# Kernel optimization log

Measured on AMD Instinct MI355X. Metric: run time of the kernel, lower is better.

## Reference

```python
import jax, jax.numpy as jnp
import numpy as np

NUM_HEADS = 8


def setup_inputs() -> dict:
    key = jax.random.key(0)
    ks = jax.random.split(key, 6)
    B, E, L = 8, 256, 4096
    top_k = 256
    return {
        "query": jax.random.normal(ks[0], (B, E, L), jnp.float32),
        "keys": jax.random.normal(ks[1], (B, E, L), jnp.float32),
        "values": jax.random.normal(ks[2], (B, E, L), jnp.float32),
        "rand_token_ind": jax.random.randint(ks[3], (B, top_k), 0, L),
        "in_proj_weight": jax.random.normal(ks[4], (3 * E, E), jnp.float32) / np.float32(np.sqrt(E)),
        "in_proj_bias": jnp.zeros((3 * E,), jnp.float32),
        "out_proj_weight": jax.random.normal(ks[5], (E, E), jnp.float32) / np.float32(np.sqrt(E)),
        "out_proj_bias": jnp.zeros((E,), jnp.float32),
        "top_k": top_k,
    }


def _forward(query, keys, values, rand_token_ind, in_proj_weight, in_proj_bias,
             out_proj_weight, out_proj_bias, top_k):
    B, E, Lq = query.shape
    # flatten(2).transpose(-1,-2): channel-first -> [B, L, E]
    q = jnp.swapaxes(query, 1, 2)
    k = jnp.swapaxes(keys, 1, 2)
    v = jnp.swapaxes(values, 1, 2)

    # --- dist_to_random_Q_selection ---
    # random subset of queries, [B, S, E]
    Q_small = jnp.take_along_axis(q, rand_token_ind[:, :, None], axis=1)

    # running min over subset queries of L1 distance (avoids [B,Lk,S,D] blowup)
    def step(min_d, qs):  # qs: [B, E]
        d = jnp.sum(jnp.abs(k - qs[:, None, :]), axis=-1)  # [B, Lk]
        return jnp.minimum(min_d, d), None

    init = jnp.full((B, k.shape[1]), jnp.inf, dtype=k.dtype)
    min_d, _ = jax.lax.scan(step, init, jnp.swapaxes(Q_small, 0, 1))

    # top_k smallest distances, sorted ascending (torch largest=False, sorted=True)
    _, idx = jax.lax.top_k(-min_d, top_k)  # idx: [B, top_k]
    sk = jnp.take_along_axis(k, idx[:, :, None], axis=1)  # [B, top_k, E]
    sv = jnp.take_along_axis(v, idx[:, :, None], axis=1)

    # --- standard torch MultiheadAttention (batch_first) ---
    Wq, Wk, Wv = jnp.split(in_proj_weight, 3, axis=0)
    bq, bk, bv = jnp.split(in_proj_bias, 3, axis=0)
    hd = E // NUM_HEADS
    scale = hd ** -0.5

    def heads(x):
        return x.reshape(x.shape[0], x.shape[1], NUM_HEADS, hd)

    qh = heads(q @ Wq.T + bq) * scale      # [B, Lq, H, hd]
    kh = heads(sk @ Wk.T + bk)             # [B, K,  H, hd]
    vh = heads(sv @ Wv.T + bv)

    scores = jnp.einsum('bqhd,bkhd->bhqk', qh, kh)
    attn = jax.nn.softmax(scores, axis=-1)
    o = jnp.einsum('bhqk,bkhd->bqhd', attn, vh).reshape(B, Lq, E)
    out = o @ out_proj_weight.T + out_proj_bias  # [B, Lq, E]

    # transpose back to original [B, E, Lq] layout
    return jnp.swapaxes(out, 1, 2)


def reference(query, keys, values, rand_token_ind, in_proj_weight, in_proj_bias,
              out_proj_weight, out_proj_bias, top_k):
    return _forward(query, keys, values, rand_token_ind, in_proj_weight,
                    in_proj_bias, out_proj_weight, out_proj_bias, top_k)
```

## Files before the change

### kernel.cpp

```cpp
#include <hip/hip_runtime.h>
#include <math.h>

#define B_SZ   8
#define E_DIM  256
#define L_SEQ  4096
#define S_TOP  256
#define NHEAD  8
#define HD     32
#define NSPLIT 4
#define JSPL   8

typedef __attribute__((ext_vector_type(8))) short bf16x8;
typedef __attribute__((ext_vector_type(4))) float f32x4;

__device__ inline short f2bf(float x) {
    union { float f; unsigned u; } v; v.f = x;
    unsigned r = (v.u + 0x7fff + ((v.u >> 16) & 1)) >> 16;
    return (short)r;
}

__global__ __launch_bounds__(256) void k_gather(const float* __restrict__ query,
                                                const int* __restrict__ ind,
                                                float* __restrict__ qs_pack) {
    int t = blockIdx.x * 256 + threadIdx.x;
    int e = t & (E_DIM - 1);
    int s = (t >> 8) & (S_TOP - 1);
    int b = t >> 16;
    int idx = ind[b * S_TOP + s];
    qs_pack[t] = query[((size_t)b * E_DIM + e) * L_SEQ + idx];
}

__global__ __launch_bounds__(256) void k_dist(const float* __restrict__ keys,
                                              const float* __restrict__ qs_pack,
                                              double* __restrict__ minpart) {
    const int b  = blockIdx.z;
    const int ss = blockIdx.y;
    const int l0 = blockIdx.x * 64;
    const int lid = threadIdx.x;
    const int tx = lid & 15;
    const int ty = lid >> 4;
    __shared__ float Ks[32][64];
    __shared__ float Qs[64][36];
    double (*red)[64] = (double(*)[64])&Ks[0][0];

    const float* kb = keys + (size_t)b * E_DIM * L_SEQ + l0;
    const float* qb = qs_pack + ((size_t)b * S_TOP + ss * 64) * E_DIM;

    double d[4][4];
#pragma unroll
    for (int i = 0; i < 4; ++i)
#pragma unroll
        for (int j = 0; j < 4; ++j) d[i][j] = 0.0;

    for (int c0 = 0; c0 < E_DIM; c0 += 32) {
        __syncthreads();
#pragma unroll
        for (int r = 0; r < 2; ++r) {
            int f4 = lid + 256 * r;
            int e  = f4 >> 4, l4 = (f4 & 15) * 4;
            *(float4*)&Ks[e][l4] = *(const float4*)(kb + (size_t)(c0 + e) * L_SEQ + l4);
            int s  = f4 >> 3, e4 = (f4 & 7) * 4;
            *(float4*)&Qs[s][e4] = *(const float4*)(qb + (size_t)s * E_DIM + c0 + e4);
        }
        __syncthreads();

        float cs[4][4] = {};
#pragma unroll
        for (int e4 = 0; e4 < 32; e4 += 4) {
            float qv[4][4];
#pragma unroll
            for (int j = 0; j < 4; ++j) {
                float4 q = *(const float4*)&Qs[ty * 4 + j][e4];
                qv[j][0] = q.x; qv[j][1] = q.y; qv[j][2] = q.z; qv[j][3] = q.w;
            }
#pragma unroll
            for (int ee = 0; ee < 4; ++ee) {
                float kv[4];
#pragma unroll
                for (int i = 0; i < 4; ++i) kv[i] = Ks[e4 + ee][tx * 4 + i];
#pragma unroll
                for (int i = 0; i < 4; ++i)
#pragma unroll
                    for (int j = 0; j < 4; ++j)
                        cs[i][j] += fabsf(kv[i] - qv[j][ee]);
            }
        }
#pragma unroll
        for (int i = 0; i < 4; ++i)
#pragma unroll
            for (int j = 0; j < 4; ++j) d[i][j] += (double)cs[i][j];
    }

    double md[4];
#pragma unroll
    for (int i = 0; i < 4; ++i) {
        double m = d[i][0];
        m = fmin(m, d[i][1]);
        m = fmin(m, d[i][2]);
        m = fmin(m, d[i][3]);
        md[i] = m;
    }
    __syncthreads();
#pragma unroll
    for (int i = 0; i < 4; ++i) red[ty][tx * 4 + i] = md[i];
    __syncthreads();
    if (lid < 64) {
        double m = red[0][lid];
#pragma unroll
        for (int t = 1; t < 16; ++t) m = fmin(m, red[t][lid]);
        minpart[((size_t)(b * NSPLIT + ss)) * L_SEQ + l0 + lid] = m;
    }
}

__global__ __launch_bounds__(256) void k_rankpart(const double* __restrict__ minpart,
                                                  int* __restrict__ rankpart) {
    const int b  = blockIdx.z;
    const int js = blockIdx.y;
    const int l  = blockIdx.x * 256 + threadIdx.x;
    __shared__ double sd[512];
    const double* mp = minpart + (size_t)b * NSPLIT * L_SEQ;
    for (int jj = threadIdx.x; jj < 512; jj += 256) {
        const int j = js * 512 + jj;
        double v = mp[j];
        v = fmin(v, mp[L_SEQ + j]);
        v = fmin(v, mp[2 * L_SEQ + j]);
        v = fmin(v, mp[3 * L_SEQ + j]);
        sd[jj] = v;
    }
    double dl = mp[l];
    dl = fmin(dl, mp[L_SEQ + l]);
    dl = fmin(dl, mp[2 * L_SEQ + l]);
    dl = fmin(dl, mp[3 * L_SEQ + l]);
    __syncthreads();
    const int jbase = js * 512;
    int rank = 0;
#pragma unroll 8
    for (int jj = 0; jj < 512; ++jj) {
        double dj = sd[jj];
        rank += (dj < dl) || (dj == dl && (jbase + jj) < l) ? 1 : 0;
    }
    rankpart[((size_t)(b * JSPL + js)) * L_SEQ + l] = rank;
}

__global__ __launch_bounds__(256) void k_sel(const int* __restrict__ rankpart,
                                             int* __restrict__ sel) {
    const int t = blockIdx.x * 256 + threadIdx.x;
    const int b = t >> 12;
    const int l = t & (L_SEQ - 1);
    int r = 0;
#pragma unroll
    for (int s = 0; s < JSPL; ++s)
        r += rankpart[((size_t)(b * JSPL + s)) * L_SEQ + l];
    if (r < S_TOP) sel[b * S_TOP + r] = l;
}

__global__ __launch_bounds__(256) void k_kvproj2(const float* __restrict__ keys,
                                                 const float* __restrict__ vals,
                                                 const int* __restrict__ sel,
                                                 const float* __restrict__ Wk,
                                                 const float* __restrict__ bk,
                                                 const float* __restrict__ Wv,
                                                 const float* __restrict__ bv,
                                                 short* __restrict__ khb,
                                                 short* __restrict__ vtb) {
    const int b  = blockIdx.z;
    const int f0 = blockIdx.x * 64;
    const int TR = blockIdx.y >> 2;
    const int k0 = (blockIdx.y & 3) * 64;
    const float* src  = TR ? vals : keys;
    const float* W    = TR ? Wv : Wk;
    const float* bias = TR ? bv : bk;
    const int tx = threadIdx.x, ty = threadIdx.y;
    const int lid = ty * 16 + tx;
    __shared__ float As[16][68];
    __shared__ float Ws[16][68];
    float c[4][4] = {};
    const float* sb = src + (size_t)b * E_DIM * L_SEQ;
    const int* selb = sel + b * S_TOP;
    for (int e0 = 0; e0 < E_DIM; e0 += 16) {
        {
            int e  = lid >> 4;
            int k4 = (lid & 15) * 4;
#pragma unroll
            for (int c2 = 0; c2 < 4; ++c2) {
                int kk = k4 + c2;
                As[e][kk] = sb[(size_t)(e0 + e) * L_SEQ + selb[k0 + kk]];
            }
        }
        {
            int f  = lid >> 2;
            int e4 = (lid & 3) * 4;
            float4 w = *(const float4*)(W + (size_t)(f0 + f) * E_DIM + e0 + e4);
            Ws[e4 + 0][f] = w.x; Ws[e4 + 1][f] = w.y;
            Ws[e4 + 2][f] = w.z; Ws[e4 + 3][f] = w.w;
        }
        __syncthreads();
#pragma unroll
        for (int e = 0; e < 16; ++e) {
            float4 a = *(const float4*)&As[e][ty * 4];
            float4 w = *(const float4*)&Ws[e][tx * 4];
            float av[4] = {a.x, a.y, a.z, a.w};
            float wv[4] = {w.x, w.y, w.z, w.w};
#pragma unroll
            for (int i = 0; i < 4; ++i)
#pragma unroll
                for (int j = 0; j < 4; ++j) c[i][j] += av[i] * wv[j];
        }
        __syncthreads();
    }
    if (TR == 0) {
#pragma unroll
        for (int i = 0; i < 4; ++i) {
            short4 o;
            o.x = f2bf(c[i][0] + bias[f0 + tx * 4 + 0]);
            o.y = f2bf(c[i][1] + bias[f0 + tx * 4 + 1]);
            o.z = f2bf(c[i][2] + bias[f0 + tx * 4 + 2]);
            o.w = f2bf(c[i][3] + bias[f0 + tx * 4 + 3]);
            *(short4*)(khb + ((size_t)b * S_TOP + k0 + ty * 4 + i) * E_DIM + f0 + tx * 4) = o;
        }
    } else {
#pragma unroll
        for (int j = 0; j < 4; ++j) {
            const float bvv = bias[f0 + tx * 4 + j];
            short4 o;
            o.x = f2bf(c[0][j] + bvv); o.y = f2bf(c[1][j] + bvv);
            o.z = f2bf(c[2][j] + bvv); o.w = f2bf(c[3][j] + bvv);
            *(short4*)(vtb + ((size_t)b * E_DIM + f0 + tx * 4 + j) * S_TOP + k0 + ty * 4) = o;
        }
    }
}

__global__ __launch_bounds__(256) void k_qproj(const float* __restrict__ query,
                                               const float* __restrict__ W,
                                               const float* __restrict__ bias,
                                               short* __restrict__ qhb,
                                               float scale) {
    const int b  = blockIdx.z;
    const int f0 = blockIdx.x * 128;
    const int l0 = blockIdx.y * 128;
    const int tx = threadIdx.x, ty = threadIdx.y;
    const int lid = ty * 16 + tx;
    __shared__ float As[16][132];
    __shared__ float Ws[16][132];
    float c[8][8] = {};
    const float* sb = query + (size_t)b * E_DIM * L_SEQ + l0;
    for (int e0 = 0; e0 < E_DIM; e0 += 16) {
        __syncthreads();
#pragma unroll
        for (int r = 0; r < 2; ++r) {
            int f4 = lid + 256 * r;
            int e  = f4 >> 5, l4 = (f4 & 31) * 4;
            *(float4*)&As[e][l4] = *(const float4*)(sb + (size_t)(e0 + e) * L_SEQ + l4);
            int f  = f4 >> 2, e4 = (f4 & 3) * 4;
            float4 w = *(const float4*)(W + (size_t)(f0 + f) * E_DIM + e0 + e4);
            Ws[e4 + 0][f] = w.x; Ws[e4 + 1][f] = w.y;
            Ws[e4 + 2][f] = w.z; Ws[e4 + 3][f] = w.w;
        }
        __syncthreads();
#pragma unroll
        for (int e = 0; e < 16; ++e) {
            float4 a0 = *(const float4*)&As[e][tx * 4];
            float4 a1 = *(const float4*)&As[e][64 + tx * 4];
            float4 w0 = *(const float4*)&Ws[e][ty * 4];
            float4 w1 = *(const float4*)&Ws[e][64 + ty * 4];
            float av[8] = {a0.x, a0.y, a0.z, a0.w, a1.x, a1.y, a1.z, a1.w};
            float wv[8] = {w0.x, w0.y, w0.z, w0.w, w1.x, w1.y, w1.z, w1.w};
#pragma unroll
            for (int i = 0; i < 8; ++i)
#pragma unroll
                for (int j = 0; j < 8; ++j) c[i][j] += av[i] * wv[j];
        }
    }
    float bv[8];
#pragma unroll
    for (int j = 0; j < 8; ++j)
        bv[j] = bias[f0 + ((j < 4) ? ty * 4 + j : 64 + ty * 4 + (j - 4))];
#pragma unroll
    for (int i = 0; i < 8; ++i) {
        const int l = l0 + ((i < 4) ? tx * 4 + i : 64 + tx * 4 + (i - 4));
        short* row = qhb + ((size_t)b * L_SEQ + l) * E_DIM + f0;
        short4 o0, o1;
        o0.x = f2bf(scale * (c[i][0] + bv[0]));
        o0.y = f2bf(scale * (c[i][1] + bv[1]));
        o0.z = f2bf(scale * (c[i][2] + bv[2]));
        o0.w = f2bf(scale * (c[i][3] + bv[3]));
        o1.x = f2bf(scale * (c[i][4] + bv[4]));
        o1.y = f2bf(scale * (c[i][5] + bv[5]));
        o1.z = f2bf(scale * (c[i][6] + bv[6]));
        o1.w = f2bf(scale * (c[i][7] + bv[7]));
        *(short4*)(row + ty * 4) = o0;
        *(short4*)(row + 64 + ty * 4) = o1;
    }
}

__global__ __launch_bounds__(256) void k_attn(const short* __restrict__ qhb,
                                              const short* __restrict__ khb,
                                              const short* __restrict__ vtb,
                                              float* __restrict__ ob) {
    __shared__ short P[4][16][264];
    const int b = blockIdx.z, h = blockIdx.y;
    const int wv   = threadIdx.x >> 6;
    const int lane = threadIdx.x & 63;
    const int quad = lane >> 4;
    const int m    = lane & 15;
    const int l0 = blockIdx.x * 64 + wv * 16;

    const short* qp = qhb + ((size_t)b * L_SEQ + l0 + m) * E_DIM + h * HD + quad * 8;
    const bf16x8 qa = *(const bf16x8*)qp;

    const short* kb = khb + (size_t)b * S_TOP * E_DIM + h * HD + quad * 8;
    f32x4 sacc[16];
    const f32x4 zero = {0.f, 0.f, 0.f, 0.f};
#pragma unroll
    for (int t = 0; t < 16; ++t) {
        bf16x8 kf = *(const bf16x8*)(kb + (size_t)(t * 16 + m) * E_DIM);
        sacc[t] = __builtin_amdgcn_mfma_f32_16x16x32_bf16(qa, kf, zero, 0, 0, 0);
    }

    float mx[4], ssum[4];
#pragma unroll
    for (int r = 0; r < 4; ++r) {
        float v = sacc[0][r];
#pragma unroll
        for (int t = 1; t < 16; ++t) v = fmaxf(v, sacc[t][r]);
#pragma unroll
        for (int off = 1; off < 16; off <<= 1) v = fmaxf(v, __shfl_xor(v, off, 16));
        mx[r] = v;
        ssum[r] = 0.f;
    }
#pragma unroll
    for (int t = 0; t < 16; ++t) {
#pragma unroll
        for (int r = 0; r < 4; ++r) {
            float p = __expf(sacc[t][r] - mx[r]);
            ssum[r] += p;
            P[wv][quad * 4 + r][t * 16 + m] = f2bf(p);
        }
    }
#pragma unroll
    for (int r = 0; r < 4; ++r) {
        float v = ssum[r];
#pragma unroll
        for (int off = 1; off < 16; off <<= 1) v += __shfl_xor(v, off, 16);
        ssum[r] = v;
    }

    const short* vb = vtb + ((size_t)b * E_DIM + h * HD) * S_TOP;
    f32x4 oacc[2];
#pragma unroll
    for (int dt = 0; dt < 2; ++dt) {
        f32x4 acc = zero;
#pragma unroll
        for (int k0 = 0; k0 < S_TOP; k0 += 32) {
            bf16x8 pa = *(const bf16x8*)&P[wv][m][k0 + quad * 8];
            bf16x8 vf = *(const bf16x8*)(vb + (size_t)(dt * 16 + m) * S_TOP + k0 + quad * 8);
            acc = __builtin_amdgcn_mfma_f32_16x16x32_bf16(pa, vf, acc, 0, 0, 0);
        }
        oacc[dt] = acc;
    }

    float* op = ob + ((size_t)b * L_SEQ + l0) * E_DIM + h * HD;
#pragma unroll
    for (int r = 0; r < 4; ++r) {
        const float inv = 1.0f / ssum[r];
#pragma unroll
        for (int dt = 0; dt < 2; ++dt)
            op[(size_t)(quad * 4 + r) * E_DIM + dt * 16 + m] = oacc[dt][r] * inv;
    }
}

__global__ __launch_bounds__(256) void k_outproj(const float* __restrict__ ob,
                                                 const float* __restrict__ W,
                                                 const float* __restrict__ bias,
                                                 float* __restrict__ out) {
    const int b  = blockIdx.z;
    const int l0 = blockIdx.x * 128;
    const int f0 = blockIdx.y * 128;
    const int tx = threadIdx.x, ty = threadIdx.y;
    const int lid = ty * 16 + tx;
    __shared__ float As[16][132];
    __shared__ float Ws[16][132];
    float c[8][8] = {};
    const float* sb = ob + (size_t)b * L_SEQ * E_DIM;
    for (int e0 = 0; e0 < E_DIM; e0 += 16) {
        __syncthreads();
#pragma unroll
        for (int r = 0; r < 2; ++r) {
            int f4 = lid + 256 * r;
            int l  = f4 >> 2, e4 = (f4 & 3) * 4;
            float4 a = *(const float4*)(sb + (size_t)(l0 + l) * E_DIM + e0 + e4);
            As[e4 + 0][l] = a.x; As[e4 + 1][l] = a.y;
            As[e4 + 2][l] = a.z; As[e4 + 3][l] = a.w;
            float4 w = *(const float4*)(W + (size_t)(f0 + l) * E_DIM + e0 + e4);
            Ws[e4 + 0][l] = w.x; Ws[e4 + 1][l] = w.y;
            Ws[e4 + 2][l] = w.z; Ws[e4 + 3][l] = w.w;
        }
        __syncthreads();
#pragma unroll
        for (int e = 0; e < 16; ++e) {
            float4 a0 = *(const float4*)&As[e][tx * 4];
            float4 a1 = *(const float4*)&As[e][64 + tx * 4];
            float4 w0 = *(const float4*)&Ws[e][ty * 4];
            float4 w1 = *(const float4*)&Ws[e][64 + ty * 4];
            float av[8] = {a0.x, a0.y, a0.z, a0.w, a1.x, a1.y, a1.z, a1.w};
            float wv[8] = {w0.x, w0.y, w0.z, w0.w, w1.x, w1.y, w1.z, w1.w};
#pragma unroll
            for (int i = 0; i < 8; ++i)
#pragma unroll
                for (int j = 0; j < 8; ++j) c[i][j] += wv[i] * av[j];
        }
    }
#pragma unroll
    for (int i = 0; i < 8; ++i) {
        const int f = f0 + ((i < 4) ? ty * 4 + i : 64 + ty * 4 + (i - 4));
        const float bvv = bias[f];
        float* row = out + ((size_t)b * E_DIM + f) * L_SEQ + l0;
        float4 o0, o1;
        o0.x = c[i][0] + bvv; o0.y = c[i][1] + bvv;
        o0.z = c[i][2] + bvv; o0.w = c[i][3] + bvv;
        o1.x = c[i][4] + bvv; o1.y = c[i][5] + bvv;
        o1.z = c[i][6] + bvv; o1.w = c[i][7] + bvv;
        *(float4*)(row + tx * 4) = o0;
        *(float4*)(row + 64 + tx * 4) = o1;
    }
}

extern "C" void kernel_launch(void* const* d_in, const int* in_sizes, int n_in,
                              void* d_out, int out_size, void* d_ws, size_t ws_size,
                              hipStream_t stream) {
    const float* query = (const float*)d_in[0];
    const float* keys  = (const float*)d_in[1];
    const float* vals  = (const float*)d_in[2];
    const int*   rind  = (const int*)d_in[3];
    const float* ipw   = (const float*)d_in[4];
    const float* ipb   = (const float*)d_in[5];
    const float* opw   = (const float*)d_in[6];
    const float* opb   = (const float*)d_in[7];
    float* out = (float*)d_out;

    char* ws = (char*)d_ws;
    float*  qs_pack  = (float*)(ws + 0);
    double* minpart  = (double*)(ws + (size_t)2  * 1024 * 1024);
    int*    sel      = (int*)   (ws + (size_t)3  * 1024 * 1024);
    short*  khb      = (short*) (ws + (size_t)4  * 1024 * 1024);
    int*    rankpart = (int*)   (ws + (size_t)5  * 1024 * 1024);
    short*  vtb      = (short*) (ws + (size_t)6  * 1024 * 1024);
    short*  qhb      = (short*) (ws + (size_t)8  * 1024 * 1024);
    float*  obuf     = (float*) (ws + (size_t)40 * 1024 * 1024);

    const float scale = 0.17677669529663687f;

    k_gather<<<dim3((B_SZ * E_DIM * S_TOP) / 256), 256, 0, stream>>>(query, rind, qs_pack);
    k_dist<<<dim3(L_SEQ / 64, NSPLIT, B_SZ), dim3(256), 0, stream>>>(keys, qs_pack, minpart);
    k_rankpart<<<dim3(L_SEQ / 256, JSPL, B_SZ), 256, 0, stream>>>(minpart, rankpart);
    k_sel<<<dim3((B_SZ * L_SEQ) / 256), 256, 0, stream>>>(rankpart, sel);
    k_kvproj2<<<dim3(E_DIM / 64, 2 * (S_TOP / 64), B_SZ), dim3(16, 16), 0, stream>>>(
        keys, vals, sel,
        ipw + (size_t)E_DIM * E_DIM, ipb + E_DIM,
        ipw + (size_t)2 * E_DIM * E_DIM, ipb + 2 * E_DIM,
        khb, vtb);
    k_qproj<<<dim3(E_DIM / 128, L_SEQ / 128, B_SZ), dim3(16, 16), 0, stream>>>(
        query, ipw, ipb, qhb, scale);
    k_attn<<<dim3(L_SEQ / 64, NHEAD, B_SZ), 256, 0, stream>>>(qhb, khb, vtb, obuf);
    k_outproj<<<dim3(L_SEQ / 128, E_DIM / 128, B_SZ), dim3(16, 16), 0, stream>>>(
        obuf, opw, opb, out);
}
```

Measured before the change: 495.4 us.

## Move Q and output projections to split-bf16 MFMA GEMMs

Replaces the fp32 SIMT tiled GEMMs for the Q projection and output projection with bf16 MFMA kernels. Accuracy is kept by splitting each fp32 operand into a hi and a lo bf16 part and summing three products (hi*hi, hi*lo, lo*hi). New conversion kernels transpose the query and split it and the weights into hi/lo parts. The attention kernel now writes its output directly as hi/lo bf16 instead of fp32. This trades an extra conversion pass and more memory traffic for much higher matrix throughput.

```diff
diff --git a/kernel.cpp b/kernel.cpp
--- a/kernel.cpp
+++ b/kernel.cpp
@@ -17,6 +17,10 @@
     union { float f; unsigned u; } v; v.f = x;
     unsigned r = (v.u + 0x7fff + ((v.u >> 16) & 1)) >> 16;
     return (short)r;
+}
+__device__ inline float bf2f(short h) {
+    union { unsigned u; float f; } c; c.u = ((unsigned)(unsigned short)h) << 16;
+    return c.f;
 }
 
 __global__ __launch_bounds__(256) void k_gather(const float* __restrict__ query,
@@ -230,73 +234,155 @@
     }
 }
 
-__global__ __launch_bounds__(256) void k_qproj(const float* __restrict__ query,
-                                               const float* __restrict__ W,
+__global__ __launch_bounds__(256) void k_wconv(const float* __restrict__ wq,
+                                               const float* __restrict__ wo,
+                                               short* __restrict__ wqhi,
+                                               short* __restrict__ wqlo,
+                                               short* __restrict__ wohi,
+                                               short* __restrict__ wolo) {
+    int t = blockIdx.x * 256 + threadIdx.x;
+    float xq = wq[t];
+    short hq = f2bf(xq);
+    wqhi[t] = hq;
+    wqlo[t] = f2bf(xq - bf2f(hq));
+    float xo = wo[t];
+    short ho = f2bf(xo);
+    wohi[t] = ho;
+    wolo[t] = f2bf(xo - bf2f(ho));
+}
+
+__global__ __launch_bounds__(256) void k_qconv(const float* __restrict__ query,
+                                               short* __restrict__ qhi,
+                                               short* __restrict__ qlo) {
+    const int b  = blockIdx.z;
+    const int e0 = blockIdx.y * 64;
+    const int l0 = blockIdx.x * 64;
+    __shared__ float T[64][68];
+    const float* src = query + ((size_t)b * E_DIM + e0) * L_SEQ + l0;
+#pragma unroll
+    for (int r = 0; r < 4; ++r) {
+        int idx = threadIdx.x + 256 * r;
+        int e = idx >> 4, l4 = (idx & 15) * 4;
+        *(float4*)&T[e][l4] = *(const float4*)(src + (size_t)e * L_SEQ + l4);
+    }
+    __syncthreads();
+    const int l  = threadIdx.x >> 2;
+    const int ec = (threadIdx.x & 3) * 16;
+    size_t dst = ((size_t)b * L_SEQ + l0 + l) * E_DIM + e0 + ec;
+    bf16x8 h0, h1, lo0, lo1;
+#pragma unroll
+    for (int k = 0; k < 8; ++k) {
+        float x = T[ec + k][l];
+        short h = f2bf(x);
+        h0[k] = h; lo0[k] = f2bf(x - bf2f(h));
+    }
+#pragma unroll
+    for (int k = 0; k < 8; ++k) {
+        float x = T[ec + 8 + k][l];
+        short h = f2bf(x);
+        h1[k] = h; lo1[k] = f2bf(x - bf2f(h));
+    }
+    *(bf16x8*)(qhi + dst)     = h0;
+    *(bf16x8*)(qhi + dst + 8) = h1;
+    *(bf16x8*)(qlo + dst)     = lo0;
+    *(bf16x8*)(qlo + dst + 8) = lo1;
+}
+
+__global__ __launch_bounds__(256) void k_qgemm(const short* __restrict__ qhi,
+                                               const short* __restrict__ qlo,
+                                               const short* __restrict__ wqhi,
+                                               const short* __restrict__ wqlo,
                                                const float* __restrict__ bias,
                                                short* __restrict__ qhb,
                                                float scale) {
     const int b  = blockIdx.z;
     const int f0 = blockIdx.x * 128;
     const int l0 = blockIdx.y * 128;
-    const int tx = threadIdx.x, ty = threadIdx.y;
-    const int lid = ty * 16 + tx;
-    __shared__ float As[16][132];
-    __shared__ float Ws[16][132];
-    float c[8][8] = {};
-    const float* sb = query + (size_t)b * E_DIM * L_SEQ + l0;
-    for (int e0 = 0; e0 < E_DIM; e0 += 16) {
+    const int lid  = threadIdx.x;
+    const int wv   = lid >> 6;
+    const int lane = lid & 63;
+    const int quad = lane >> 4;
+    const int m    = lane & 15;
+    const int wf   = wv >> 1;
+    const int wl   = wv & 1;
+
+    __shared__ short Awh[128 * 40];
+    __shared__ short Awl[128 * 40];
+    __shared__ short Bqh[128 * 40];
+    __shared__ short Bql[128 * 40];
+
+    const short* wh_g = wqhi + (size_t)f0 * E_DIM;
+    const short* wl_g = wqlo + (size_t)f0 * E_DIM;
+    const short* qh_g = qhi + ((size_t)b * L_SEQ + l0) * E_DIM;
+    const short* ql_g = qlo + ((size_t)b * L_SEQ + l0) * E_DIM;
+
+    f32x4 acc[4][4];
+    const f32x4 zero = {0.f, 0.f, 0.f, 0.f};
+#pragma unroll
+    for (int i = 0; i < 4; ++i)
+#pragma unroll
+        for (int j = 0; j < 4; ++j) acc[i][j] = zero;
+
+    for (int k0 = 0; k0 < E_DIM; k0 += 32) {
         __syncthreads();
 #pragma unroll
         for (int r = 0; r < 2; ++r) {
-            int f4 = lid + 256 * r;
-            int e  = f4 >> 5, l4 = (f4 & 31) * 4;
-            *(float4*)&As[e][l4] = *(const float4*)(sb + (size_t)(e0 + e) * L_SEQ + l4);
-            int f  = f4 >> 2, e4 = (f4 & 3) * 4;
-            float4 w = *(const float4*)(W + (size_t)(f0 + f) * E_DIM + e0 + e4);
-            Ws[e4 + 0][f] = w.x; Ws[e4 + 1][f] = w.y;
-            Ws[e4 + 2][f] = w.z; Ws[e4 + 3][f] = w.w;
-        }
-        __syncthreads();
-#pragma unroll
-        for (int e = 0; e < 16; ++e) {
-            float4 a0 = *(const float4*)&As[e][tx * 4];
-            float4 a1 = *(const float4*)&As[e][64 + tx * 4];
-            float4 w0 = *(const float4*)&Ws[e][ty * 4];
-            float4 w1 = *(const float4*)&Ws[e][64 + ty * 4];
-            float av[8] = {a0.x, a0.y, a0.z, a0.w, a1.x, a1.y, a1.z, a1.w};
-            float wv[8] = {w0.x, w0.y, w0.z, w0.w, w1.x, w1.y, w1.z, w1.w};
-#pragma unroll
-            for (int i = 0; i < 8; ++i)
-#pragma unroll
-                for (int j = 0; j < 8; ++j) c[i][j] += av[i] * wv[j];
-        }
-    }
-    float bv[8];
-#pragma unroll
-    for (int j = 0; j < 8; ++j)
-        bv[j] = bias[f0 + ((j < 4) ? ty * 4 + j : 64 + ty * 4 + (j - 4))];
-#pragma unroll
-    for (int i = 0; i < 8; ++i) {
-        const int l = l0 + ((i < 4) ? tx * 4 + i : 64 + tx * 4 + (i - 4));
-        short* row = qhb + ((size_t)b * L_SEQ + l) * E_DIM + f0;
-        short4 o0, o1;
-        o0.x = f2bf(scale * (c[i][0] + bv[0]));
-        o0.y = f2bf(scale * (c[i][1] + bv[1]));
-        o0.z = f2bf(scale * (c[i][2] + bv[2]));
-        o0.w = f2bf(scale * (c[i][3] + bv[3]));
-        o1.x = f2bf(scale * (c[i][4] + bv[4]));
-        o1.y = f2bf(scale * (c[i][5] + bv[5]));
-        o1.z = f2bf(scale * (c[i][6] + bv[6]));
-        o1.w = f2bf(scale * (c[i][7] + bv[7]));
-        *(short4*)(row + ty * 4) = o0;
-        *(short4*)(row + 64 + ty * 4) = o1;
+            int idx = lid + 256 * r;
+            int row = idx >> 2;
+            int kc  = (idx & 3) * 8;
+            *(bf16x8*)&Awh[row * 40 + kc] = *(const bf16x8*)(wh_g + (size_t)row * E_DIM + k0 + kc);
+            *(bf16x8*)&Awl[row * 40 + kc] = *(const bf16x8*)(wl_g + (size_t)row * E_DIM + k0 + kc);
+            *(bf16x8*)&Bqh[row * 40 + kc] = *(const bf16x8*)(qh_g + (size_t)row * E_DIM + k0 + kc);
+            *(bf16x8*)&Bql[row * 40 + kc] = *(const bf16x8*)(ql_g + (size_t)row * E_DIM + k0 + kc);
+        }
+        __syncthreads();
+
+        bf16x8 ah[4], al[4], bh[4], bl[4];
+#pragma unroll
+        for (int tf = 0; tf < 4; ++tf) {
+            int row = wf * 64 + tf * 16 + m;
+            ah[tf] = *(const bf16x8*)&Awh[row * 40 + quad * 8];
+            al[tf] = *(const bf16x8*)&Awl[row * 40 + quad * 8];
+        }
+#pragma unroll
+        for (int tl = 0; tl < 4; ++tl) {
+            int row = wl * 64 + tl * 16 + m;
+            bh[tl] = *(const bf16x8*)&Bqh[row * 40 + quad * 8];
+            bl[tl] = *(const bf16x8*)&Bql[row * 40 + quad * 8];
+        }
+#pragma unroll
+        for (int tf = 0; tf < 4; ++tf)
+#pragma unroll
+            for (int tl = 0; tl < 4; ++tl) {
+                acc[tf][tl] = __builtin_amdgcn_mfma_f32_16x16x32_bf16(al[tf], bh[tl], acc[tf][tl], 0, 0, 0);
+                acc[tf][tl] = __builtin_amdgcn_mfma_f32_16x16x32_bf16(ah[tf], bl[tl], acc[tf][tl], 0, 0, 0);
+                acc[tf][tl] = __builtin_amdgcn_mfma_f32_16x16x32_bf16(ah[tf], bh[tl], acc[tf][tl], 0, 0, 0);
+            }
+    }
+
+#pragma unroll
+    for (int tf = 0; tf < 4; ++tf) {
+        const int fb = f0 + wf * 64 + tf * 16 + quad * 4;
+        float bv0 = bias[fb + 0], bv1 = bias[fb + 1];
+        float bv2 = bias[fb + 2], bv3 = bias[fb + 3];
+#pragma unroll
+        for (int tl = 0; tl < 4; ++tl) {
+            const int l = l0 + wl * 64 + tl * 16 + m;
+            short4 o;
+            o.x = f2bf(scale * (acc[tf][tl][0] + bv0));
+            o.y = f2bf(scale * (acc[tf][tl][1] + bv1));
+            o.z = f2bf(scale * (acc[tf][tl][2] + bv2));
+            o.w = f2bf(scale * (acc[tf][tl][3] + bv3));
+            *(short4*)(qhb + ((size_t)b * L_SEQ + l) * E_DIM + fb) = o;
+        }
     }
 }
 
 __global__ __launch_bounds__(256) void k_attn(const short* __restrict__ qhb,
                                               const short* __restrict__ khb,
                                               const short* __restrict__ vtb,
-                                              float* __restrict__ ob) {
+                                              short* __restrict__ ohi,
+                                              short* __restrict__ olo) {
     __shared__ short P[4][16][264];
     const int b = blockIdx.z, h = blockIdx.y;
     const int wv   = threadIdx.x >> 6;
@@ -359,69 +445,107 @@
         oacc[dt] = acc;
     }
 
-    float* op = ob + ((size_t)b * L_SEQ + l0) * E_DIM + h * HD;
+    short* oph = ohi + ((size_t)b * L_SEQ + l0) * E_DIM + h * HD;
+    short* opl = olo + ((size_t)b * L_SEQ + l0) * E_DIM + h * HD;
 #pragma unroll
     for (int r = 0; r < 4; ++r) {
         const float inv = 1.0f / ssum[r];
 #pragma unroll
-        for (int dt = 0; dt < 2; ++dt)
-            op[(size_t)(quad * 4 + r) * E_DIM + dt * 16 + m] = oacc[dt][r] * inv;
-    }
-}
-
-__global__ __launch_bounds__(256) void k_outproj(const float* __restrict__ ob,
-                                                 const float* __restrict__ W,
-                                                 const float* __restrict__ bias,
-                                                 float* __restrict__ out) {
+        for (int dt = 0; dt < 2; ++dt) {
+            float val = oacc[dt][r] * inv;
+            short hh = f2bf(val);
+            size_t off = (size_t)(quad * 4 + r) * E_DIM + dt * 16 + m;
+            oph[off] = hh;
+            opl[off] = f2bf(val - bf2f(hh));
+        }
+    }
+}
+
+__global__ __launch_bounds__(256) void k_ogemm(const short* __restrict__ ohi,
+                                               const short* __restrict__ olo,
+                                               const short* __restrict__ wohi,
+                                               const short* __restrict__ wolo,
+                                               const float* __restrict__ bias,
+                                               float* __restrict__ out) {
     const int b  = blockIdx.z;
-    const int l0 = blockIdx.x * 128;
-    const int f0 = blockIdx.y * 128;
-    const int tx = threadIdx.x, ty = threadIdx.y;
-    const int lid = ty * 16 + tx;
-    __shared__ float As[16][132];
-    __shared__ float Ws[16][132];
-    float c[8][8] = {};
-    const float* sb = ob + (size_t)b * L_SEQ * E_DIM;
-    for (int e0 = 0; e0 < E_DIM; e0 += 16) {
+    const int f0 = blockIdx.x * 128;
+    const int l0 = blockIdx.y * 128;
+    const int lid  = threadIdx.x;
+    const int wv   = lid >> 6;
+    const int lane = lid & 63;
+    const int quad = lane >> 4;
+    const int m    = lane & 15;
+    const int wl   = wv >> 1;
+    const int wf   = wv & 1;
+
+    __shared__ short Aoh[128 * 40];
+    __shared__ short Aol[128 * 40];
+    __shared__ short Bwh[128 * 40];
+    __shared__ short Bwl[128 * 40];
+
+    const short* oh_g = ohi + ((size_t)b * L_SEQ + l0) * E_DIM;
+    const short* ol_g = olo + ((size_t)b * L_SEQ + l0) * E_DIM;
+    const short* wh_g = wohi + (size_t)f0 * E_DIM;
+    const short* wl_g = wolo + (size_t)f0 * E_DIM;
+
+    f32x4 acc[4][4];
+    const f32x4 zero = {0.f, 0.f, 0.f, 0.f};
+#pragma unroll
+    for (int i = 0; i < 4; ++i)
+#pragma unroll
+        for (int j = 0; j < 4; ++j) acc[i][j] = zero;
+
+    for (int k0 = 0; k0 < E_DIM; k0 += 32) {
         __syncthreads();
 #pragma unroll
         for (int r = 0; r < 2; ++r) {
-            int f4 = lid + 256 * r;
-            int l  = f4 >> 2, e4 = (f4 & 3) * 4;
-            float4 a = *(const float4*)(sb + (size_t)(l0 + l) * E_DIM + e0 + e4);
-            As[e4 + 0][l] = a.x; As[e4 + 1][l] = a.y;
-            As[e4 + 2][l] = a.z; As[e4 + 3][l] = a.w;
-            float4 w = *(const float4*)(W + (size_t)(f0 + l) * E_DIM + e0 + e4);
-            Ws[e4 + 0][l] = w.x; Ws[e4 + 1][l] = w.y;
-            Ws[e4 + 2][l] = w.z; Ws[e4 + 3][l] = w.w;
-        }
-        __syncthreads();
-#pragma unroll
-        for (int e = 0; e < 16; ++e) {
-            float4 a0 = *(const float4*)&As[e][tx * 4];
-            float4 a1 = *(const float4*)&As[e][64 + tx * 4];
-            float4 w0 = *(const float4*)&Ws[e][ty * 4];
-            float4 w1 = *(const float4*)&Ws[e][64 + ty * 4];
-            float av[8] = {a0.x, a0.y, a0.z, a0.w, a1.x, a1.y, a1.z, a1.w};
-            float wv[8] = {w0.x, w0.y, w0.z, w0.w, w1.x, w1.y, w1.z, w1.w};
-#pragma unroll
-            for (int i = 0; i < 8; ++i)
-#pragma unroll
-                for (int j = 0; j < 8; ++j) c[i][j] += wv[i] * av[j];
-        }
-    }
-#pragma unroll
-    for (int i = 0; i < 8; ++i) {
-        const int f = f0 + ((i < 4) ? ty * 4 + i : 64 + ty * 4 + (i - 4));
-        const float bvv = bias[f];
-        float* row = out + ((size_t)b * E_DIM + f) * L_SEQ + l0;
-        float4 o0, o1;
-        o0.x = c[i][0] + bvv; o0.y = c[i][1] + bvv;
-        o0.z = c[i][2] + bvv; o0.w = c[i][3] + bvv;
-        o1.x = c[i][4] + bvv; o1.y = c[i][5] + bvv;
-        o1.z = c[i][6] + bvv; o1.w = c[i][7] + bvv;
-        *(float4*)(row + tx * 4) = o0;
-        *(float4*)(row + 64 + tx * 4) = o1;
+            int idx = lid + 256 * r;
+            int row = idx >> 2;
+            int kc  = (idx & 3) * 8;
+            *(bf16x8*)&Aoh[row * 40 + kc] = *(const bf16x8*)(oh_g + (size_t)row * E_DIM + k0 + kc);
+            *(bf16x8*)&Aol[row * 40 + kc] = *(const bf16x8*)(ol_g + (size_t)row * E_DIM + k0 + kc);
+            *(bf16x8*)&Bwh[row * 40 + kc] = *(const bf16x8*)(wh_g + (size_t)row * E_DIM + k0 + kc);
+            *(bf16x8*)&Bwl[row * 40 + kc] = *(const bf16x8*)(wl_g + (size_t)row * E_DIM + k0 + kc);
+        }
+        __syncthreads();
+
+        bf16x8 ah[4], al[4], bh[4], bl[4];
+#pragma unroll
+        for (int tl = 0; tl < 4; ++tl) {
+            int row = wl * 64 + tl * 16 + m;
+            ah[tl] = *(const bf16x8*)&Aoh[row * 40 + quad * 8];
+            al[tl] = *(const bf16x8*)&Aol[row * 40 + quad * 8];
+        }
+#pragma unroll
+        for (int tf = 0; tf < 4; ++tf) {
+            int row = wf * 64 + tf * 16 + m;
+            bh[tf] = *(const bf16x8*)&Bwh[row * 40 + quad * 8];
+            bl[tf] = *(const bf16x8*)&Bwl[row * 40 + quad * 8];
+        }
+#pragma unroll
+        for (int tl = 0; tl < 4; ++tl)
+#pragma unroll
+            for (int tf = 0; tf < 4; ++tf) {
+                acc[tl][tf] = __builtin_amdgcn_mfma_f32_16x16x32_bf16(al[tl], bh[tf], acc[tl][tf], 0, 0, 0);
+                acc[tl][tf] = __builtin_amdgcn_mfma_f32_16x16x32_bf16(ah[tl], bl[tf], acc[tl][tf], 0, 0, 0);
+                acc[tl][tf] = __builtin_amdgcn_mfma_f32_16x16x32_bf16(ah[tl], bh[tf], acc[tl][tf], 0, 0, 0);
+            }
+    }
+
+#pragma unroll
+    for (int tl = 0; tl < 4; ++tl) {
+        const int lb = l0 + wl * 64 + tl * 16 + quad * 4;
+#pragma unroll
+        for (int tf = 0; tf < 4; ++tf) {
+            const int f = f0 + wf * 64 + tf * 16 + m;
+            const float bv = bias[f];
+            float4 o;
+            o.x = acc[tl][tf][0] + bv;
+            o.y = acc[tl][tf][1] + bv;
+            o.z = acc[tl][tf][2] + bv;
+            o.w = acc[tl][tf][3] + bv;
+            *(float4*)(out + ((size_t)b * E_DIM + f) * L_SEQ + lb) = o;
+        }
     }
 }
 
@@ -439,14 +563,22 @@
     float* out = (float*)d_out;
 
     char* ws = (char*)d_ws;
+    const size_t MI = 1024 * 1024;
     float*  qs_pack  = (float*)(ws + 0);
-    double* minpart  = (double*)(ws + (size_t)2  * 1024 * 1024);
-    int*    sel      = (int*)   (ws + (size_t)3  * 1024 * 1024);
-    short*  khb      = (short*) (ws + (size_t)4  * 1024 * 1024);
-    int*    rankpart = (int*)   (ws + (size_t)5  * 1024 * 1024);
-    short*  vtb      = (short*) (ws + (size_t)6  * 1024 * 1024);
-    short*  qhb      = (short*) (ws + (size_t)8  * 1024 * 1024);
-    float*  obuf     = (float*) (ws + (size_t)40 * 1024 * 1024);
+    double* minpart  = (double*)(ws + 2 * MI);
+    int*    sel      = (int*)   (ws + 3 * MI);
+    short*  khb      = (short*) (ws + 4 * MI);
+    int*    rankpart = (int*)   (ws + 5 * MI);
+    short*  vtb      = (short*) (ws + 6 * MI);
+    short*  wqhi     = (short*) (ws + 7 * MI);
+    short*  wqlo     = (short*) (ws + 7 * MI + 131072);
+    short*  wohi     = (short*) (ws + 7 * MI + 2 * 131072);
+    short*  wolo     = (short*) (ws + 7 * MI + 3 * 131072);
+    short*  qhb      = (short*) (ws + 8 * MI);
+    short*  qhi      = (short*) (ws + 24 * MI);
+    short*  qlo      = (short*) (ws + 40 * MI);
+    short*  ohi      = (short*) (ws + 24 * MI);
+    short*  olo      = (short*) (ws + 40 * MI);
 
     const float scale = 0.17677669529663687f;
 
@@ -459,9 +591,11 @@
         ipw + (size_t)E_DIM * E_DIM, ipb + E_DIM,
         ipw + (size_t)2 * E_DIM * E_DIM, ipb + 2 * E_DIM,
         khb, vtb);
-    k_qproj<<<dim3(E_DIM / 128, L_SEQ / 128, B_SZ), dim3(16, 16), 0, stream>>>(
-        query, ipw, ipb, qhb, scale);
-    k_attn<<<dim3(L_SEQ / 64, NHEAD, B_SZ), 256, 0, stream>>>(qhb, khb, vtb, obuf);
-    k_outproj<<<dim3(L_SEQ / 128, E_DIM / 128, B_SZ), dim3(16, 16), 0, stream>>>(
-        obuf, opw, opb, out);
-}
+    k_wconv<<<dim3(256), 256, 0, stream>>>(ipw, opw, wqhi, wqlo, wohi, wolo);
+    k_qconv<<<dim3(L_SEQ / 64, E_DIM / 64, B_SZ), 256, 0, stream>>>(query, qhi, qlo);
+    k_qgemm<<<dim3(E_DIM / 128, L_SEQ / 128, B_SZ), 256, 0, stream>>>(
+        qhi, qlo, wqhi, wqlo, ipb, qhb, scale);
+    k_attn<<<dim3(L_SEQ / 64, NHEAD, B_SZ), 256, 0, stream>>>(qhb, khb, vtb, ohi, olo);
+    k_ogemm<<<dim3(E_DIM / 128, L_SEQ / 128, B_SZ), 256, 0, stream>>>(
+        ohi, olo, wohi, wolo, opb, out);
+}
```

New measurement: 440.0 us. -11.2%, faster.
